# Kernel optimization log

Hardware: AMD Instinct MI355X
Metric: run time of the kernel (lower is better)

## Reference

```python
import jax, jax.numpy as jnp
import numpy as np
from jax import lax

B, N, C = 4, 9216, 64
HH = WW = 96
SR = 2
NUM_HEADS = 1
EPS = 1e-5


def setup_inputs() -> dict:
    key = jax.random.key(0)
    ks = jax.random.split(key, 8)
    w = 0.05  # keep logits in a stable range
    return {
        "x": jax.random.normal(ks[0], (B, N, C), jnp.float32),
        "conv_w": jax.random.normal(ks[1], (C, C, SR, SR), jnp.float32) * w,
        "conv_b": jnp.zeros((C,), jnp.float32),
        "bn_gamma": jnp.ones((C,), jnp.float32),
        "bn_beta": jnp.zeros((C,), jnp.float32),
        "bn_mean": jnp.zeros((C,), jnp.float32),
        "bn_var": jnp.ones((C,), jnp.float32),
        "ln_gamma": jnp.ones((C,), jnp.float32),
        "ln_beta": jnp.zeros((C,), jnp.float32),
        "wq": jax.random.normal(ks[2], (C, C), jnp.float32) * w,
        "wkv": jax.random.normal(ks[3], (2 * C, C), jnp.float32) * w,
        "wproj": jax.random.normal(ks[4], (C, C), jnp.float32) * w,
        "bproj": jnp.zeros((C,), jnp.float32),
        "H": HH,
        "W": WW,
    }


def reference(x, conv_w, conv_b, bn_gamma, bn_beta, bn_mean, bn_var,
              ln_gamma, ln_beta, wq, wkv, wproj, bproj, H, W):
    b, n, c = x.shape
    hd = c // NUM_HEADS
    scale = c ** (-0.5)  # torch uses full dim for the scale

    # q projection: [B, heads, N, hd]
    q = (x @ wq.T).reshape(b, n, NUM_HEADS, hd).transpose(0, 2, 1, 3)

    # spatial reduce: conv(stride=SR, kernel=SR) + BN (inference stats)
    x_ = x.transpose(0, 2, 1).reshape(b, c, H, W)
    x_ = lax.conv_general_dilated(x_, conv_w, (SR, SR), 'VALID',
                                  dimension_numbers=('NCHW', 'OIHW', 'NCHW'))
    x_ = x_ + conv_b[None, :, None, None]
    x_ = (x_ - bn_mean[None, :, None, None]) * lax.rsqrt(bn_var + EPS)[None, :, None, None]
    x_ = x_ * bn_gamma[None, :, None, None] + bn_beta[None, :, None, None]
    x_ = x_.reshape(b, c, -1).transpose(0, 2, 1)  # [B, N', C]

    # LayerNorm over channel dim
    mu = jnp.mean(x_, axis=-1, keepdims=True)
    var = jnp.var(x_, axis=-1, keepdims=True)
    x_ = (x_ - mu) * lax.rsqrt(var + EPS) * ln_gamma + ln_beta

    # kv projection: [2, B, heads, N', hd]
    kv = (x_ @ wkv.T).reshape(b, -1, 2, NUM_HEADS, hd).transpose(2, 0, 3, 1, 4)
    k, v = kv[0], kv[1]

    attn = jnp.einsum('bhnd,bhmd->bhnm', q, k) * scale  # [B,h,N,N']
    attn = jax.nn.softmax(attn, axis=-1)
    out = jnp.einsum('bhnm,bhmd->bhnd', attn, v)
    out = out.transpose(0, 2, 1, 3).reshape(b, n, c)
    return out @ wproj.T + bproj
```

## Files before the change

kernel.cpp:

```cpp
#include <hip/hip_runtime.h>

#define NB   4
#define NQ   9216
#define NKV  2304
#define NSPL 4
#define KSPL 576
#define EPS  1e-5f

typedef __attribute__((ext_vector_type(8))) short          short8;
typedef __attribute__((ext_vector_type(8))) unsigned short ushort8;
typedef __attribute__((ext_vector_type(4))) unsigned short ushort4v;
typedef __attribute__((ext_vector_type(4))) unsigned int   uint4v;
typedef __attribute__((ext_vector_type(4))) float          f32x4;

static __device__ __forceinline__ f32x4 mfma_bf16(ushort8 a, ushort8 b, f32x4 c) {
    return __builtin_amdgcn_mfma_f32_16x16x32_bf16(
        __builtin_bit_cast(short8, a), __builtin_bit_cast(short8, b), c, 0, 0, 0);
}

static __device__ __forceinline__ unsigned short f2bf(float f) {
    unsigned int u = __float_as_uint(f);
    u = (u + 0x7fffu + ((u >> 16) & 1u)) >> 16;
    return (unsigned short)u;
}
static __device__ __forceinline__ float bf2f(unsigned short u) {
    return __uint_as_float(((unsigned int)u) << 16);
}
static __device__ __forceinline__ ushort4v pack4(f32x4 v) {
    ushort4v r; r.x = f2bf(v.x); r.y = f2bf(v.y); r.z = f2bf(v.z); r.w = f2bf(v.w);
    return r;
}
static __device__ __forceinline__ unsigned int cvt_pk_bf16(float lo, float hi) {
    unsigned int r;
    asm("v_cvt_pk_bf16_f32 %0, %1, %2" : "=v"(r) : "v"(lo), "v"(hi));
    return r;
}

#define QSCALE 0.18033688011112042f

__global__ __launch_bounds__(256) void prep_fused_kernel(
    const float* __restrict__ x, const float* __restrict__ conv_w,
    const float* __restrict__ conv_b, const float* __restrict__ bn_g,
    const float* __restrict__ bn_b, const float* __restrict__ bn_m,
    const float* __restrict__ bn_v, const float* __restrict__ ln_g,
    const float* __restrict__ ln_b, const float* __restrict__ wkv,
    const float* __restrict__ wq, const float* __restrict__ wproj,
    unsigned short* __restrict__ Kb, unsigned short* __restrict__ VTb,
    unsigned short* __restrict__ qb, unsigned short* __restrict__ wpb)
{
    __shared__ __align__(16) unsigned char ldsraw[20608];
    const int tid = threadIdx.x;

    if (blockIdx.x >= 1152) {
        const float4* s = (const float4*)(wproj + tid * 16);
        const float4 f0 = s[0], f1 = s[1], f2 = s[2], f3 = s[3];
        ushort8 a, b;
        a[0]=f2bf(f0.x); a[1]=f2bf(f0.y); a[2]=f2bf(f0.z); a[3]=f2bf(f0.w);
        a[4]=f2bf(f1.x); a[5]=f2bf(f1.y); a[6]=f2bf(f1.z); a[7]=f2bf(f1.w);
        b[0]=f2bf(f2.x); b[1]=f2bf(f2.y); b[2]=f2bf(f2.z); b[3]=f2bf(f2.w);
        b[4]=f2bf(f3.x); b[5]=f2bf(f3.y); b[6]=f2bf(f3.z); b[7]=f2bf(f3.w);
        *(ushort8*)(wpb + tid * 16)     = a;
        *(ushort8*)(wpb + tid * 16 + 8) = b;
        return;
    }

    if (blockIdx.x >= 576) {
        unsigned short* xbT = (unsigned short*)ldsraw;
        unsigned short* wqb = xbT + 4608;
        const long tok0 = (long)(blockIdx.x - 576) * 64;
        {
            const int tok = tid >> 2, c0 = (tid & 3) * 16;
            const float4* s = (const float4*)(x + (tok0 + tok) * 64 + c0);
            const float4 f0 = s[0], f1 = s[1], f2 = s[2], f3 = s[3];
            ushort8 a, b;
            a[0]=f2bf(f0.x); a[1]=f2bf(f0.y); a[2]=f2bf(f0.z); a[3]=f2bf(f0.w);
            a[4]=f2bf(f1.x); a[5]=f2bf(f1.y); a[6]=f2bf(f1.z); a[7]=f2bf(f1.w);
            b[0]=f2bf(f2.x); b[1]=f2bf(f2.y); b[2]=f2bf(f2.z); b[3]=f2bf(f2.w);
            b[4]=f2bf(f3.x); b[5]=f2bf(f3.y); b[6]=f2bf(f3.z); b[7]=f2bf(f3.w);
            *(ushort8*)(xbT + tok * 72 + c0)     = a;
            *(ushort8*)(xbT + tok * 72 + c0 + 8) = b;
            const float4* ws = (const float4*)(wq + tid * 16);
            const float4 g0 = ws[0], g1 = ws[1], g2 = ws[2], g3 = ws[3];
            ushort8 c, d;
            c[0]=f2bf(g0.x*QSCALE); c[1]=f2bf(g0.y*QSCALE); c[2]=f2bf(g0.z*QSCALE); c[3]=f2bf(g0.w*QSCALE);
            c[4]=f2bf(g1.x*QSCALE); c[5]=f2bf(g1.y*QSCALE); c[6]=f2bf(g1.z*QSCALE); c[7]=f2bf(g1.w*QSCALE);
            d[0]=f2bf(g2.x*QSCALE); d[1]=f2bf(g2.y*QSCALE); d[2]=f2bf(g2.z*QSCALE); d[3]=f2bf(g2.w*QSCALE);
            d[4]=f2bf(g3.x*QSCALE); d[5]=f2bf(g3.y*QSCALE); d[6]=f2bf(g3.z*QSCALE); d[7]=f2bf(g3.w*QSCALE);
            *(ushort8*)(wqb + tok * 72 + c0)     = c;
            *(ushort8*)(wqb + tok * 72 + c0 + 8) = d;
        }
        __syncthreads();
        const int w = tid >> 6, i = tid & 15, g = (tid >> 4) & 3;
        const ushort8 xb0 = *(const ushort8*)(xbT + (w * 16 + i) * 72 + g * 8);
        const ushort8 xb1 = *(const ushort8*)(xbT + (w * 16 + i) * 72 + 32 + g * 8);
        const f32x4 zero = {0.f, 0.f, 0.f, 0.f};
#pragma unroll
        for (int ot = 0; ot < 4; ++ot) {
            const ushort8 a0 = *(const ushort8*)(wqb + (ot * 16 + i) * 72 + g * 8);
            const ushort8 a1 = *(const ushort8*)(wqb + (ot * 16 + i) * 72 + 32 + g * 8);
            f32x4 acc = mfma_bf16(a0, xb0, zero);
            acc = mfma_bf16(a1, xb1, acc);
            *(ushort4v*)(qb + (tok0 + w * 16 + i) * 64 + ot * 16 + g * 4) = pack4(acc);
        }
        return;
    }

    float*  xs    = (float*)ldsraw;
    float*  ys    = (float*)(ldsraw + 16384);
    float2* stats = (float2*)(ldsraw + 20480);
    const int b  = blockIdx.x / 144;
    const int p0 = (blockIdx.x % 144) * 16;
    {
        const int r = tid >> 2, kk = tid & 3;
        const int tok = r >> 2, pix = r & 3;
        const int p = p0 + tok;
        const int i = p / 48, j = p - i * 48;
        const int n = (2 * i + (pix >> 1)) * 96 + 2 * j + (pix & 1);
        const float* src = x + ((long)b * NQ + n) * 64 + kk * 16;
#pragma unroll
        for (int cc = 0; cc < 4; ++cc) {
            const float4 v = *(const float4*)(src + cc * 4);
            const int c = kk * 16 + cc * 4;
            xs[(c + 0) * 64 + r] = v.x;
            xs[(c + 1) * 64 + r] = v.y;
            xs[(c + 2) * 64 + r] = v.z;
            xs[(c + 3) * 64 + r] = v.w;
        }
    }
    __syncthreads();
    const int o = tid & 63, tg = tid >> 6;
    {
        float a0 = 0.f, a1 = 0.f, a2 = 0.f, a3 = 0.f;
        const float4* wrow = (const float4*)(conv_w + (long)o * 256);
        const float* xbase = xs + tg * 16;
#pragma unroll 8
        for (int c = 0; c < 64; ++c) {
            const float4 w4 = wrow[c];
            const float* xr = xbase + c * 64;
            const float4 x0 = *(const float4*)(xr + 0);
            const float4 x1 = *(const float4*)(xr + 4);
            const float4 x2 = *(const float4*)(xr + 8);
            const float4 x3 = *(const float4*)(xr + 12);
            a0 += w4.x * x0.x + w4.y * x0.y + w4.z * x0.z + w4.w * x0.w;
            a1 += w4.x * x1.x + w4.y * x1.y + w4.z * x1.z + w4.w * x1.w;
            a2 += w4.x * x2.x + w4.y * x2.y + w4.z * x2.z + w4.w * x2.w;
            a3 += w4.x * x3.x + w4.y * x3.y + w4.z * x3.z + w4.w * x3.w;
        }
        const float rs = rsqrtf(bn_v[o] + EPS);
        const float sh = conv_b[o] - bn_m[o];
        const float gg = bn_g[o], bb = bn_b[o];
        ys[(tg * 4 + 0) * 64 + o] = (a0 + sh) * rs * gg + bb;
        ys[(tg * 4 + 1) * 64 + o] = (a1 + sh) * rs * gg + bb;
        ys[(tg * 4 + 2) * 64 + o] = (a2 + sh) * rs * gg + bb;
        ys[(tg * 4 + 3) * 64 + o] = (a3 + sh) * rs * gg + bb;
    }
    __syncthreads();
    {
        const int tk = tid >> 4, s = tid & 15;
        const float4 yv = *(const float4*)(ys + tk * 64 + s * 4);
        float s1 = yv.x + yv.y + yv.z + yv.w;
        float s2 = yv.x * yv.x + yv.y * yv.y + yv.z * yv.z + yv.w * yv.w;
#pragma unroll
        for (int mm = 1; mm <= 8; mm <<= 1) {
            s1 += __shfl_xor(s1, mm);
            s2 += __shfl_xor(s2, mm);
        }
        if (s == 0) {
            const float mu = s1 * (1.f / 64.f);
            const float var = s2 * (1.f / 64.f) - mu * mu;
            stats[tk] = make_float2(mu, rsqrtf(var + EPS));
        }
    }
    __syncthreads();
    {
        const float lg = ln_g[o], lb = ln_b[o];
#pragma unroll
        for (int qq = 0; qq < 4; ++qq) {
            const int tt = tg * 4 + qq;
            const float2 st = stats[tt];
            ys[tt * 64 + o] = (ys[tt * 64 + o] - st.x) * st.y * lg + lb;
        }
    }
    __syncthreads();
    {
        float k0 = 0.f, k1 = 0.f, k2 = 0.f, k3 = 0.f;
        float v0 = 0.f, v1 = 0.f, v2 = 0.f, v3 = 0.f;
        const float4* wkr = (const float4*)(wkv + (long)o * 64);
        const float4* wvr = (const float4*)(wkv + (long)(64 + o) * 64);
        const float* zbase = ys + tg * 256;
#pragma unroll
        for (int c4 = 0; c4 < 16; ++c4) {
            const float4 wk = wkr[c4], wv = wvr[c4];
            const float4 z0 = *(const float4*)(zbase + 0 * 64 + c4 * 4);
            const float4 z1 = *(const float4*)(zbase + 1 * 64 + c4 * 4);
            const float4 z2 = *(const float4*)(zbase + 2 * 64 + c4 * 4);
            const float4 z3 = *(const float4*)(zbase + 3 * 64 + c4 * 4);
            k0 += wk.x * z0.x + wk.y * z0.y + wk.z * z0.z + wk.w * z0.w;
            k1 += wk.x * z1.x + wk.y * z1.y + wk.z * z1.z + wk.w * z1.w;
            k2 += wk.x * z2.x + wk.y * z2.y + wk.z * z2.z + wk.w * z2.w;
            k3 += wk.x * z3.x + wk.y * z3.y + wk.z * z3.z + wk.w * z3.w;
            v0 += wv.x * z0.x + wv.y * z0.y + wv.z * z0.z + wv.w * z0.w;
            v1 += wv.x * z1.x + wv.y * z1.y + wv.z * z1.z + wv.w * z1.w;
            v2 += wv.x * z2.x + wv.y * z2.y + wv.z * z2.z + wv.w * z2.w;
            v3 += wv.x * z3.x + wv.y * z3.y + wv.z * z3.z + wv.w * z3.w;
        }
        const long pg = (long)b * NKV + p0 + tg * 4;
        Kb[(pg + 0) * 64 + o] = f2bf(k0);
        Kb[(pg + 1) * 64 + o] = f2bf(k1);
        Kb[(pg + 2) * 64 + o] = f2bf(k2);
        Kb[(pg + 3) * 64 + o] = f2bf(k3);
        unsigned short* vt = VTb + ((long)b * 64 + o) * NKV + p0 + tg * 4;
        vt[0] = f2bf(v0); vt[1] = f2bf(v1); vt[2] = f2bf(v2); vt[3] = f2bf(v3);
    }
}

__global__ __launch_bounds__(256, 8) void attn_kernel(
    const unsigned short* __restrict__ qb, const unsigned short* __restrict__ Kb,
    const unsigned short* __restrict__ VTb, unsigned short* __restrict__ Opart,
    float* __restrict__ Ml)
{
    __shared__ __align__(16) unsigned short smem[9728];
    unsigned short* ldsK  = smem;
    unsigned short* ldsVT = smem + 4608;

    const int tid  = threadIdx.x;
    const int lane = tid & 63;
    const int lq = lane & 15;
    const int g  = lane >> 4;
    const int s   = blockIdx.x / 576;
    const int rem = blockIdx.x % 576;
    const int b   = rem / 144;
    const int q0  = (rem % 144) * 64 + (tid >> 6) * 16;
    const int kbase = s * KSPL;

    const unsigned short* qrow = qb + ((long)b * NQ + q0 + lq) * 64 + g * 8;
    const ushort8 qf0 = *(const ushort8*)qrow;
    const ushort8 qf1 = *(const ushort8*)(qrow + 32);

    const int kr   = tid >> 3;
    const int slot = (((kr >> 2) & 1) << 4) + ((kr >> 3) << 2) + (kr & 3);
    const unsigned short* gK  = Kb  + ((long)b * NKV + kbase + kr) * 64 + (tid & 7) * 8;
    const unsigned short* gVT = VTb + ((long)b * 64 + (tid >> 2)) * NKV + kbase + (tid & 3) * 8;
    const int lkw = slot * 72 + (tid & 7) * 8;
    const int lvw = (tid >> 2) * 40 + (tid & 3) * 8;

    float lsum = 0.f;
    const f32x4 zero = {0.f, 0.f, 0.f, 0.f};
    f32x4 oa0 = zero, oa1 = zero, oa2 = zero, oa3 = zero;

    ushort8 rk = *(const ushort8*)gK;
    ushort8 rv = *(const ushort8*)gVT;
    *(ushort8*)(ldsK + lkw)  = rk;
    *(ushort8*)(ldsVT + lvw) = rv;
    __syncthreads();

    for (int t = 0; t < 18; ++t) {
        const unsigned short* K_ = ldsK  + (t & 1) * 2304;
        const unsigned short* V_ = ldsVT + (t & 1) * 2560;
        if (t < 17) {
            rk = *(const ushort8*)(gK + (long)(t + 1) * 2048);
            rv = *(const ushort8*)(gVT + (t + 1) * 32);
        }
        f32x4 s0 = zero, s1 = zero;
        {
            const ushort8 a0 = *(const ushort8*)(K_ + lq * 72 + g * 8);
            const ushort8 a1 = *(const ushort8*)(K_ + lq * 72 + 32 + g * 8);
            const ushort8 a2 = *(const ushort8*)(K_ + (16 + lq) * 72 + g * 8);
            const ushort8 a3 = *(const ushort8*)(K_ + (16 + lq) * 72 + 32 + g * 8);
            s0 = mfma_bf16(a0, qf0, s0);
            s0 = mfma_bf16(a1, qf1, s0);
            s1 = mfma_bf16(a2, qf0, s1);
            s1 = mfma_bf16(a3, qf1, s1);
        }
        f32x4 e0, e1;
        e0.x = __builtin_amdgcn_exp2f(s0.x); e0.y = __builtin_amdgcn_exp2f(s0.y);
        e0.z = __builtin_amdgcn_exp2f(s0.z); e0.w = __builtin_amdgcn_exp2f(s0.w);
        e1.x = __builtin_amdgcn_exp2f(s1.x); e1.y = __builtin_amdgcn_exp2f(s1.y);
        e1.z = __builtin_amdgcn_exp2f(s1.z); e1.w = __builtin_amdgcn_exp2f(s1.w);
        lsum += ((e0.x + e0.y) + (e0.z + e0.w)) + ((e1.x + e1.y) + (e1.z + e1.w));
        uint4v pw;
        pw.x = cvt_pk_bf16(e0.x, e0.y);
        pw.y = cvt_pk_bf16(e0.z, e0.w);
        pw.z = cvt_pk_bf16(e1.x, e1.y);
        pw.w = cvt_pk_bf16(e1.z, e1.w);
        const ushort8 pf = __builtin_bit_cast(ushort8, pw);
        {
            const ushort8 v0 = *(const ushort8*)(V_ + lq * 40 + g * 8);
            const ushort8 v1 = *(const ushort8*)(V_ + (16 + lq) * 40 + g * 8);
            const ushort8 v2 = *(const ushort8*)(V_ + (32 + lq) * 40 + g * 8);
            const ushort8 v3 = *(const ushort8*)(V_ + (48 + lq) * 40 + g * 8);
            oa0 = mfma_bf16(v0, pf, oa0);
            oa1 = mfma_bf16(v1, pf, oa1);
            oa2 = mfma_bf16(v2, pf, oa2);
            oa3 = mfma_bf16(v3, pf, oa3);
        }
        if (t < 17) {
            *(ushort8*)(ldsK + ((t + 1) & 1) * 2304 + lkw)  = rk;
            *(ushort8*)(ldsVT + ((t + 1) & 1) * 2560 + lvw) = rv;
        }
        __syncthreads();
    }

    float tot = lsum;
    tot += __shfl_xor(tot, 16);
    tot += __shfl_xor(tot, 32);
    const float inv = 1.f / tot;
    oa0 = oa0 * inv; oa1 = oa1 * inv; oa2 = oa2 * inv; oa3 = oa3 * inv;
    const long obase = (((long)s * NB + b) * NQ + q0 + lq) * 64;
    *(ushort4v*)(Opart + obase + 0  + g * 4) = pack4(oa0);
    *(ushort4v*)(Opart + obase + 16 + g * 4) = pack4(oa1);
    *(ushort4v*)(Opart + obase + 32 + g * 4) = pack4(oa2);
    *(ushort4v*)(Opart + obase + 48 + g * 4) = pack4(oa3);
    if (g == 0) Ml[((long)s * NB + b) * NQ + q0 + lq] = tot;
}

__global__ __launch_bounds__(256) void combine_kernel(
    const unsigned short* __restrict__ Opart, const float* __restrict__ Ml,
    const unsigned short* __restrict__ wpb, const float* __restrict__ bproj,
    float* __restrict__ out)
{
    __shared__ unsigned short pe[4][16 * 72];
    const int tid = threadIdx.x;
    const int w = tid >> 6, lq = tid & 15, g = (tid >> 4) & 3;
    const int b  = blockIdx.x / 144;
    const int q0 = (blockIdx.x % 144) * 64;
    const long q = (long)q0 + w * 16 + lq;

    float wt[NSPL], wsum = 0.f;
#pragma unroll
    for (int sp = 0; sp < NSPL; ++sp) {
        wt[sp] = Ml[((long)sp * NB + b) * NQ + q];
        wsum += wt[sp];
    }
    float acc[16];
#pragma unroll
    for (int j = 0; j < 16; ++j) acc[j] = 0.f;
#pragma unroll
    for (int sp = 0; sp < NSPL; ++sp) {
        const unsigned short* op = Opart + (((long)sp * NB + b) * NQ + q) * 64 + g * 16;
        const ushort8 u0 = *(const ushort8*)op;
        const ushort8 u1 = *(const ushort8*)(op + 8);
        const float wg = wt[sp];
#pragma unroll
        for (int j = 0; j < 8; ++j) acc[j]     += wg * bf2f(u0[j]);
#pragma unroll
        for (int j = 0; j < 8; ++j) acc[8 + j] += wg * bf2f(u1[j]);
    }
    const float sc = 1.f / wsum;
    ushort8 e0, e1;
#pragma unroll
    for (int j = 0; j < 8; ++j) { e0[j] = f2bf(acc[j] * sc); e1[j] = f2bf(acc[8 + j] * sc); }
    unsigned short* pew = pe[w];
    *(ushort8*)(pew + lq * 72 + g * 16)     = e0;
    *(ushort8*)(pew + lq * 72 + g * 16 + 8) = e1;
    const ushort8 af0 = *(const ushort8*)(pew + lq * 72 + g * 8);
    const ushort8 af1 = *(const ushort8*)(pew + lq * 72 + 32 + g * 8);
    const f32x4 zero = {0.f, 0.f, 0.f, 0.f};
#pragma unroll
    for (int et = 0; et < 4; ++et) {
        const unsigned short* wr = wpb + (et * 16 + lq) * 64 + g * 8;
        const ushort8 w0 = *(const ushort8*)wr;
        const ushort8 w1 = *(const ushort8*)(wr + 32);
        f32x4 acc2 = mfma_bf16(af0, w0, zero);
        acc2 = mfma_bf16(af1, w1, acc2);
        const float bias = bproj[et * 16 + lq];
        float* orow = out + ((long)b * NQ + q0 + w * 16 + 4 * g) * 64 + et * 16 + lq;
        orow[0]   = acc2.x + bias;
        orow[64]  = acc2.y + bias;
        orow[128] = acc2.z + bias;
        orow[192] = acc2.w + bias;
    }
}

extern "C" void kernel_launch(void* const* d_in, const int* in_sizes, int n_in,
                              void* d_out, int out_size, void* d_ws, size_t ws_size,
                              hipStream_t stream)
{
    (void)in_sizes; (void)n_in; (void)out_size; (void)ws_size;
    const float* x      = (const float*)d_in[0];
    const float* conv_w = (const float*)d_in[1];
    const float* conv_b = (const float*)d_in[2];
    const float* bn_g   = (const float*)d_in[3];
    const float* bn_b   = (const float*)d_in[4];
    const float* bn_m   = (const float*)d_in[5];
    const float* bn_v   = (const float*)d_in[6];
    const float* ln_g   = (const float*)d_in[7];
    const float* ln_b   = (const float*)d_in[8];
    const float* wq     = (const float*)d_in[9];
    const float* wkv    = (const float*)d_in[10];
    const float* wproj  = (const float*)d_in[11];
    const float* bpr    = (const float*)d_in[12];

    unsigned short* qb    = (unsigned short*)d_ws;
    unsigned short* Kb    = qb + 2359296;
    unsigned short* VTb   = Kb + 589824;
    unsigned short* wpb   = VTb + 589824;
    unsigned short* Opart = wpb + 4096;
    float*          Ml    = (float*)(Opart + 9437184);

    prep_fused_kernel<<<1153, 256, 0, stream>>>(x, conv_w, conv_b, bn_g, bn_b, bn_m,
                                                bn_v, ln_g, ln_b, wkv, wq, wproj,
                                                Kb, VTb, qb, wpb);
    attn_kernel<<<2304, 256, 0, stream>>>(qb, Kb, VTb, Opart, Ml);
    combine_kernel<<<576, 256, 0, stream>>>(Opart, Ml, wpb, bpr, (float*)d_out);
}
```

Before: 173.8 us.

## Switch attention to 32x32x16 MFMA tiles and pre-transpose conv/kv weights

The attention kernel now has each wave handle 32 query rows using 32x32x16 bf16 MFMAs, so each block covers 128 queries and the grid is halved. This reuses each K/V tile read from LDS across more queries and lowers the instruction count per score, at the cost of more accumulator registers (launch bounds cut from 8 to 5 blocks). A new small kernel transposes the conv and kv weights so that threads in a wave read weights with coalesced float4 loads. The K LDS slot permutation is changed to match the new fragment layout.

New measurement: 149.6 us. -14.0%, faster.

```diff
diff --git a/kernel.cpp b/kernel.cpp
--- a/kernel.cpp
+++ b/kernel.cpp
@@ -7,14 +7,19 @@
 #define KSPL 576
 #define EPS  1e-5f
 
-typedef __attribute__((ext_vector_type(8))) short          short8;
-typedef __attribute__((ext_vector_type(8))) unsigned short ushort8;
-typedef __attribute__((ext_vector_type(4))) unsigned short ushort4v;
-typedef __attribute__((ext_vector_type(4))) unsigned int   uint4v;
-typedef __attribute__((ext_vector_type(4))) float          f32x4;
-
-static __device__ __forceinline__ f32x4 mfma_bf16(ushort8 a, ushort8 b, f32x4 c) {
+typedef __attribute__((ext_vector_type(8)))  short          short8;
+typedef __attribute__((ext_vector_type(8)))  unsigned short ushort8;
+typedef __attribute__((ext_vector_type(4)))  unsigned short ushort4v;
+typedef __attribute__((ext_vector_type(4)))  unsigned int   uint4v;
+typedef __attribute__((ext_vector_type(4)))  float          f32x4;
+typedef __attribute__((ext_vector_type(16))) float          f32x16;
+
+static __device__ __forceinline__ f32x4 mfma16(ushort8 a, ushort8 b, f32x4 c) {
     return __builtin_amdgcn_mfma_f32_16x16x32_bf16(
+        __builtin_bit_cast(short8, a), __builtin_bit_cast(short8, b), c, 0, 0, 0);
+}
+static __device__ __forceinline__ f32x16 mfma32(ushort8 a, ushort8 b, f32x16 c) {
+    return __builtin_amdgcn_mfma_f32_32x32x16_bf16(
         __builtin_bit_cast(short8, a), __builtin_bit_cast(short8, b), c, 0, 0, 0);
 }
 
@@ -38,13 +43,30 @@
 
 #define QSCALE 0.18033688011112042f
 
+__global__ __launch_bounds__(256) void prep_wt_kernel(
+    const float* __restrict__ conv_w, const float* __restrict__ wkv,
+    float* __restrict__ Wt2, float* __restrict__ Wkt2, float* __restrict__ Wvt2)
+{
+    const int idx = blockIdx.x * 256 + threadIdx.x;
+    if (idx < 16384) {
+        const int c = idx >> 8, r = idx & 255, o = r >> 2, pix = r & 3;
+        Wt2[idx] = conv_w[o * 256 + c * 4 + pix];
+    } else {
+        const int i = idx - 16384;
+        const int c4 = i >> 8, r = i & 255, o = r >> 2, j = r & 3;
+        if (c4 < 16) Wkt2[c4 * 256 + o * 4 + j] = wkv[o * 64 + c4 * 4 + j];
+        else         Wvt2[(c4 - 16) * 256 + o * 4 + j] = wkv[(64 + o) * 64 + (c4 - 16) * 4 + j];
+    }
+}
+
 __global__ __launch_bounds__(256) void prep_fused_kernel(
-    const float* __restrict__ x, const float* __restrict__ conv_w,
+    const float* __restrict__ x, const float* __restrict__ Wt2,
     const float* __restrict__ conv_b, const float* __restrict__ bn_g,
     const float* __restrict__ bn_b, const float* __restrict__ bn_m,
     const float* __restrict__ bn_v, const float* __restrict__ ln_g,
-    const float* __restrict__ ln_b, const float* __restrict__ wkv,
-    const float* __restrict__ wq, const float* __restrict__ wproj,
+    const float* __restrict__ ln_b, const float* __restrict__ Wkt2,
+    const float* __restrict__ Wvt2, const float* __restrict__ wq,
+    const float* __restrict__ wproj,
     unsigned short* __restrict__ Kb, unsigned short* __restrict__ VTb,
     unsigned short* __restrict__ qb, unsigned short* __restrict__ wpb)
 {
@@ -98,8 +120,8 @@
         for (int ot = 0; ot < 4; ++ot) {
             const ushort8 a0 = *(const ushort8*)(wqb + (ot * 16 + i) * 72 + g * 8);
             const ushort8 a1 = *(const ushort8*)(wqb + (ot * 16 + i) * 72 + 32 + g * 8);
-            f32x4 acc = mfma_bf16(a0, xb0, zero);
-            acc = mfma_bf16(a1, xb1, acc);
+            f32x4 acc = mfma16(a0, xb0, zero);
+            acc = mfma16(a1, xb1, acc);
             *(ushort4v*)(qb + (tok0 + w * 16 + i) * 64 + ot * 16 + g * 4) = pack4(acc);
         }
         return;
@@ -131,11 +153,10 @@
     const int o = tid & 63, tg = tid >> 6;
     {
         float a0 = 0.f, a1 = 0.f, a2 = 0.f, a3 = 0.f;
-        const float4* wrow = (const float4*)(conv_w + (long)o * 256);
         const float* xbase = xs + tg * 16;
 #pragma unroll 8
         for (int c = 0; c < 64; ++c) {
-            const float4 w4 = wrow[c];
+            const float4 w4 = *(const float4*)(Wt2 + c * 256 + o * 4);
             const float* xr = xbase + c * 64;
             const float4 x0 = *(const float4*)(xr + 0);
             const float4 x1 = *(const float4*)(xr + 4);
@@ -185,12 +206,11 @@
     {
         float k0 = 0.f, k1 = 0.f, k2 = 0.f, k3 = 0.f;
         float v0 = 0.f, v1 = 0.f, v2 = 0.f, v3 = 0.f;
-        const float4* wkr = (const float4*)(wkv + (long)o * 64);
-        const float4* wvr = (const float4*)(wkv + (long)(64 + o) * 64);
         const float* zbase = ys + tg * 256;
 #pragma unroll
         for (int c4 = 0; c4 < 16; ++c4) {
-            const float4 wk = wkr[c4], wv = wvr[c4];
+            const float4 wk = *(const float4*)(Wkt2 + c4 * 256 + o * 4);
+            const float4 wv = *(const float4*)(Wvt2 + c4 * 256 + o * 4);
             const float4 z0 = *(const float4*)(zbase + 0 * 64 + c4 * 4);
             const float4 z1 = *(const float4*)(zbase + 1 * 64 + c4 * 4);
             const float4 z2 = *(const float4*)(zbase + 2 * 64 + c4 * 4);
@@ -214,7 +234,7 @@
     }
 }
 
-__global__ __launch_bounds__(256, 8) void attn_kernel(
+__global__ __launch_bounds__(256, 5) void attn_kernel(
     const unsigned short* __restrict__ qb, const unsigned short* __restrict__ Kb,
     const unsigned short* __restrict__ VTb, unsigned short* __restrict__ Opart,
     float* __restrict__ Ml)
@@ -225,28 +245,32 @@
 
     const int tid  = threadIdx.x;
     const int lane = tid & 63;
-    const int lq = lane & 15;
-    const int g  = lane >> 4;
-    const int s   = blockIdx.x / 576;
-    const int rem = blockIdx.x % 576;
-    const int b   = rem / 144;
-    const int q0  = (rem % 144) * 64 + (tid >> 6) * 16;
+    const int q5 = lane & 31;
+    const int hi = lane >> 5;
+    const int wid = tid >> 6;
+    const int s   = blockIdx.x / 288;
+    const int rem = blockIdx.x % 288;
+    const int b   = rem / 72;
+    const int q0  = (rem % 72) * 128 + wid * 32;
     const int kbase = s * KSPL;
 
-    const unsigned short* qrow = qb + ((long)b * NQ + q0 + lq) * 64 + g * 8;
-    const ushort8 qf0 = *(const ushort8*)qrow;
-    const ushort8 qf1 = *(const ushort8*)(qrow + 32);
+    const unsigned short* qrow = qb + ((long)b * NQ + q0 + q5) * 64 + hi * 8;
+    const ushort8 qf0 = *(const ushort8*)(qrow);
+    const ushort8 qf1 = *(const ushort8*)(qrow + 16);
+    const ushort8 qf2 = *(const ushort8*)(qrow + 32);
+    const ushort8 qf3 = *(const ushort8*)(qrow + 48);
 
     const int kr   = tid >> 3;
-    const int slot = (((kr >> 2) & 1) << 4) + ((kr >> 3) << 2) + (kr & 3);
+    const int slot = (kr & ~12) | ((kr & 8) >> 1) | ((kr & 4) << 1);
     const unsigned short* gK  = Kb  + ((long)b * NKV + kbase + kr) * 64 + (tid & 7) * 8;
     const unsigned short* gVT = VTb + ((long)b * 64 + (tid >> 2)) * NKV + kbase + (tid & 3) * 8;
     const int lkw = slot * 72 + (tid & 7) * 8;
     const int lvw = (tid >> 2) * 40 + (tid & 3) * 8;
 
     float lsum = 0.f;
-    const f32x4 zero = {0.f, 0.f, 0.f, 0.f};
-    f32x4 oa0 = zero, oa1 = zero, oa2 = zero, oa3 = zero;
+    f32x16 oc0, oc1;
+#pragma unroll
+    for (int i = 0; i < 16; ++i) { oc0[i] = 0.f; oc1[i] = 0.f; }
 
     ushort8 rk = *(const ushort8*)gK;
     ushort8 rv = *(const ushort8*)gVT;
@@ -261,38 +285,36 @@
             rk = *(const ushort8*)(gK + (long)(t + 1) * 2048);
             rv = *(const ushort8*)(gVT + (t + 1) * 32);
         }
-        f32x4 s0 = zero, s1 = zero;
+        f32x16 sS;
+#pragma unroll
+        for (int i = 0; i < 16; ++i) sS[i] = 0.f;
         {
-            const ushort8 a0 = *(const ushort8*)(K_ + lq * 72 + g * 8);
-            const ushort8 a1 = *(const ushort8*)(K_ + lq * 72 + 32 + g * 8);
-            const ushort8 a2 = *(const ushort8*)(K_ + (16 + lq) * 72 + g * 8);
-            const ushort8 a3 = *(const ushort8*)(K_ + (16 + lq) * 72 + 32 + g * 8);
-            s0 = mfma_bf16(a0, qf0, s0);
-            s0 = mfma_bf16(a1, qf1, s0);
-            s1 = mfma_bf16(a2, qf0, s1);
-            s1 = mfma_bf16(a3, qf1, s1);
-        }
-        f32x4 e0, e1;
-        e0.x = __builtin_amdgcn_exp2f(s0.x); e0.y = __builtin_amdgcn_exp2f(s0.y);
-        e0.z = __builtin_amdgcn_exp2f(s0.z); e0.w = __builtin_amdgcn_exp2f(s0.w);
-        e1.x = __builtin_amdgcn_exp2f(s1.x); e1.y = __builtin_amdgcn_exp2f(s1.y);
-        e1.z = __builtin_amdgcn_exp2f(s1.z); e1.w = __builtin_amdgcn_exp2f(s1.w);
-        lsum += ((e0.x + e0.y) + (e0.z + e0.w)) + ((e1.x + e1.y) + (e1.z + e1.w));
-        uint4v pw;
-        pw.x = cvt_pk_bf16(e0.x, e0.y);
-        pw.y = cvt_pk_bf16(e0.z, e0.w);
-        pw.z = cvt_pk_bf16(e1.x, e1.y);
-        pw.w = cvt_pk_bf16(e1.z, e1.w);
-        const ushort8 pf = __builtin_bit_cast(ushort8, pw);
+            const int ar = q5 * 72 + hi * 8;
+            sS = mfma32(*(const ushort8*)(K_ + ar),      qf0, sS);
+            sS = mfma32(*(const ushort8*)(K_ + ar + 16), qf1, sS);
+            sS = mfma32(*(const ushort8*)(K_ + ar + 32), qf2, sS);
+            sS = mfma32(*(const ushort8*)(K_ + ar + 48), qf3, sS);
+        }
+        unsigned int pa[8];
+        float l0 = 0.f;
+#pragma unroll
+        for (int i = 0; i < 8; ++i) {
+            const float ea = __builtin_amdgcn_exp2f(sS[2 * i]);
+            const float eb = __builtin_amdgcn_exp2f(sS[2 * i + 1]);
+            l0 += ea + eb;
+            pa[i] = cvt_pk_bf16(ea, eb);
+        }
+        lsum += l0;
+        const uint4v w0 = {pa[0], pa[1], pa[2], pa[3]};
+        const uint4v w1 = {pa[4], pa[5], pa[6], pa[7]};
+        const ushort8 pf0 = __builtin_bit_cast(ushort8, w0);
+        const ushort8 pf1 = __builtin_bit_cast(ushort8, w1);
         {
-            const ushort8 v0 = *(const ushort8*)(V_ + lq * 40 + g * 8);
-            const ushort8 v1 = *(const ushort8*)(V_ + (16 + lq) * 40 + g * 8);
-            const ushort8 v2 = *(const ushort8*)(V_ + (32 + lq) * 40 + g * 8);
-            const ushort8 v3 = *(const ushort8*)(V_ + (48 + lq) * 40 + g * 8);
-            oa0 = mfma_bf16(v0, pf, oa0);
-            oa1 = mfma_bf16(v1, pf, oa1);
-            oa2 = mfma_bf16(v2, pf, oa2);
-            oa3 = mfma_bf16(v3, pf, oa3);
+            const int vr = q5 * 40 + hi * 8;
+            oc0 = mfma32(*(const ushort8*)(V_ + vr),             pf0, oc0);
+            oc0 = mfma32(*(const ushort8*)(V_ + vr + 16),        pf1, oc0);
+            oc1 = mfma32(*(const ushort8*)(V_ + 1280 + vr),      pf0, oc1);
+            oc1 = mfma32(*(const ushort8*)(V_ + 1280 + vr + 16), pf1, oc1);
         }
         if (t < 17) {
             *(ushort8*)(ldsK + ((t + 1) & 1) * 2304 + lkw)  = rk;
@@ -301,17 +323,19 @@
         __syncthreads();
     }
 
-    float tot = lsum;
-    tot += __shfl_xor(tot, 16);
-    tot += __shfl_xor(tot, 32);
+    const float tot = lsum + __shfl_xor(lsum, 32);
     const float inv = 1.f / tot;
-    oa0 = oa0 * inv; oa1 = oa1 * inv; oa2 = oa2 * inv; oa3 = oa3 * inv;
-    const long obase = (((long)s * NB + b) * NQ + q0 + lq) * 64;
-    *(ushort4v*)(Opart + obase + 0  + g * 4) = pack4(oa0);
-    *(ushort4v*)(Opart + obase + 16 + g * 4) = pack4(oa1);
-    *(ushort4v*)(Opart + obase + 32 + g * 4) = pack4(oa2);
-    *(ushort4v*)(Opart + obase + 48 + g * 4) = pack4(oa3);
-    if (g == 0) Ml[((long)s * NB + b) * NQ + q0 + lq] = tot;
+    unsigned short* ob = Opart + (((long)s * NB + b) * NQ + q0 + q5) * 64 + 4 * hi;
+#pragma unroll
+    for (int j = 0; j < 4; ++j) {
+        const f32x4 v0 = {oc0[4 * j] * inv, oc0[4 * j + 1] * inv,
+                          oc0[4 * j + 2] * inv, oc0[4 * j + 3] * inv};
+        const f32x4 v1 = {oc1[4 * j] * inv, oc1[4 * j + 1] * inv,
+                          oc1[4 * j + 2] * inv, oc1[4 * j + 3] * inv};
+        *(ushort4v*)(ob + 8 * j)      = pack4(v0);
+        *(ushort4v*)(ob + 32 + 8 * j) = pack4(v1);
+    }
+    if (hi == 0) Ml[((long)s * NB + b) * NQ + q0 + q5] = tot;
 }
 
 __global__ __launch_bounds__(256) void combine_kernel(
@@ -361,8 +385,8 @@
         const unsigned short* wr = wpb + (et * 16 + lq) * 64 + g * 8;
         const ushort8 w0 = *(const ushort8*)wr;
         const ushort8 w1 = *(const ushort8*)(wr + 32);
-        f32x4 acc2 = mfma_bf16(af0, w0, zero);
-        acc2 = mfma_bf16(af1, w1, acc2);
+        f32x4 acc2 = mfma16(af0, w0, zero);
+        acc2 = mfma16(af1, w1, acc2);
         const float bias = bproj[et * 16 + lq];
         float* orow = out + ((long)b * NQ + q0 + w * 16 + 4 * g) * 64 + et * 16 + lq;
         orow[0]   = acc2.x + bias;
@@ -397,10 +421,14 @@
     unsigned short* wpb   = VTb + 589824;
     unsigned short* Opart = wpb + 4096;
     float*          Ml    = (float*)(Opart + 9437184);
-
-    prep_fused_kernel<<<1153, 256, 0, stream>>>(x, conv_w, conv_b, bn_g, bn_b, bn_m,
-                                                bn_v, ln_g, ln_b, wkv, wq, wproj,
+    float*          Wt2   = Ml + 147456;
+    float*          Wkt2  = Wt2 + 16384;
+    float*          Wvt2  = Wkt2 + 4096;
+
+    prep_wt_kernel<<<96, 256, 0, stream>>>(conv_w, wkv, Wt2, Wkt2, Wvt2);
+    prep_fused_kernel<<<1153, 256, 0, stream>>>(x, Wt2, conv_b, bn_g, bn_b, bn_m,
+                                                bn_v, ln_g, ln_b, Wkt2, Wvt2, wq, wproj,
                                                 Kb, VTb, qb, wpb);
-    attn_kernel<<<2304, 256, 0, stream>>>(qb, Kb, VTb, Opart, Ml);
+    attn_kernel<<<1152, 256, 0, stream>>>(qb, Kb, VTb, Opart, Ml);
     combine_kernel<<<576, 256, 0, stream>>>(Opart, Ml, wpb, bpr, (float*)d_out);
 }
```
